# Kernel optimization log

Hardware: AMD Instinct MI355X
Metric: run time of the kernel (lower is better)

Reference implementation:

```python
import jax, jax.numpy as jnp
import numpy as np

N5, N4, N3, K = 10242, 2562, 642, 7  # icosphere node counts (levels 5,4,3), spatial kernel size
M = 32  # mchannel
EPS = 1e-8


def _sconv(x, neigh, W, b, relu=True):
    # x: [B,T,N,Cin]; neigh: [N,K] 1-ring indices; W: [K,Cin,Cout]
    xn = x[:, :, neigh, :]                        # [B,T,N,K,Cin] irregular gather
    y = jnp.einsum('btnkc,kcd->btnd', xn, W) + b  # per-node kernel contraction
    return jax.nn.relu(y) if relu else y


def _spool(x, pidx):
    # max-pool fine->coarse mesh: pidx [Ncoarse,Kp] indexes fine nodes
    return jnp.max(x[:, :, pidx, :], axis=3)


def _unpool(x, uidx):
    # coarse->fine copy: uidx [Nfine] indexes coarse nodes
    return x[:, :, uidx, :]


def _cos(f, a):
    # torch.nn.CosineSimilarity(dim=-1): dot / max(|f|*|a|, eps)
    dot = jnp.sum(f * a, axis=-1)
    nf = jnp.linalg.norm(f, axis=-1)
    na = jnp.linalg.norm(a, axis=-1)
    return dot / jnp.maximum(nf * na, EPS)


def setup_inputs() -> dict:
    key = jax.random.key(0)
    ks = jax.random.split(key, 32)
    w = lambda i, shape: jax.random.normal(ks[i], shape, jnp.float32) * 0.05
    inp = {
        'frame': jax.random.normal(ks[0], (1, 16, N5, 3), jnp.float32),
        'aem': jax.random.normal(ks[1], (1, 16, N5), jnp.float32),
        'W0f': w(2, (K, 3, M)),        'b0f': w(3, (M,)),
        'W0a': w(4, (K, 1, M)),        'b0a': w(5, (M,)),
        'W1f': w(6, (K, M, 2 * M)),    'b1f': w(7, (2 * M,)),
        'W1a': w(8, (K, M, 2 * M)),    'b1a': w(9, (2 * M,)),
        'W2f': w(10, (K, 2 * M, 4 * M)), 'b2f': w(11, (4 * M,)),
        'W2a': w(12, (K, 2 * M, 4 * M)), 'b2a': w(13, (4 * M,)),
        'W7': w(14, (K, 12 * M, 2 * M)), 'b7': w(15, (2 * M,)),
        'W8': w(16, (K, 4 * M, M)),    'b8': w(17, (M,)),
        'W9': w(18, (K, M, 1)),        'b9': w(19, (1,)),
        'neigh5': jax.random.randint(ks[20], (N5, K), 0, N5),
        'neigh4': jax.random.randint(ks[21], (N4, K), 0, N4),
        'neigh3': jax.random.randint(ks[22], (N3, K), 0, N3),
        'pool5': jax.random.randint(ks[23], (N4, K), 0, N5),
        'pool4': jax.random.randint(ks[24], (N3, K), 0, N4),
        'up4': jax.random.randint(ks[25], (N4,), 0, N3),
        'up5': jax.random.randint(ks[26], (N5,), 0, N4),
        'Tlocation': jax.random.randint(ks[27], (1, 16), 0, 16),
    }
    return inp


def reference(frame, aem, W0f, b0f, W0a, b0a, W1f, b1f, W1a, b1a, W2f, b2f,
              W2a, b2a, W7, b7, W8, b8, W9, b9,
              neigh5, neigh4, neigh3, pool5, pool4, up4, up5, Tlocation):
    a = aem[..., None]                                    # [B,T,N5,1]
    # encoder level 0 (N5)
    c0f = _sconv(frame, neigh5, W0f, b0f)
    c0a = _sconv(a, neigh5, W0a, b0a)
    p0f = _spool(c0f, pool5)
    p0a = _spool(c0a, pool5)
    m0 = _cos(c0f, c0a)[..., None]                        # [B,T,N5,1]
    c0f_att, c0a_att = c0f * m0, c0a * m0
    # encoder level 1 (N4)
    c1f = _sconv(p0f, neigh4, W1f, b1f)
    c1a = _sconv(p0a, neigh4, W1a, b1a)
    p1f = _spool(c1f, pool4)
    p1a = _spool(c1a, pool4)
    m1 = _cos(c1f, c1a)[..., None]
    c1f_att, c1a_att = c1f * m1, c1a * m1
    # bottleneck (N3)
    c2f = _sconv(p1f, neigh3, W2f, b2f)
    c2a = _sconv(p1a, neigh3, W2a, b2a)
    m2 = _cos(c2f, c2a)[..., None]
    conv2 = jnp.concatenate((c2f * m2, c2a * m2), axis=-1)  # [B,T,N3,8M]
    # decoder
    cat7 = jnp.concatenate((_unpool(conv2, up4), c1f_att, c1a_att), axis=-1)  # [B,T,N4,12M]
    conv7 = _sconv(cat7, neigh4, W7, b7)
    cat8 = jnp.concatenate((_unpool(conv7, up5), c0f_att, c0a_att), axis=-1)  # [B,T,N5,4M]
    conv8 = _sconv(cat8, neigh5, W8, b8)
    conv9 = _sconv(conv8, neigh5, W9, b9, relu=False)[..., 0]  # [B,T,N5]
    return jax.nn.softmax(conv9, axis=-1)
```

## Files before the change

kernel.cpp:

```cpp
#include <hip/hip_runtime.h>
#include <cfloat>
#include <cstdint>


constexpr int T  = 16;
constexpr int n5 = 10242, n4 = 2562, n3 = 642;
constexpr int K  = 7;

using bf16x8 = __attribute__((ext_vector_type(8))) short;
using f32x4  = __attribute__((ext_vector_type(4))) float;

static __device__ __forceinline__ float bf2f(unsigned short u) {
    return __uint_as_float((unsigned)u << 16);
}
static __device__ __forceinline__ unsigned short f2bf(float x) {
    unsigned u = __float_as_uint(x);
    u += 0x7FFF + ((u >> 16) & 1);
    return (unsigned short)(u >> 16);
}

__global__ __launch_bounds__(256) void conv0_kernel(
    const float* __restrict__ frame, const float* __restrict__ aem,
    const float* __restrict__ W0f, const float* __restrict__ b0f,
    const float* __restrict__ W0a, const float* __restrict__ b0a,
    const int* __restrict__ neigh5,
    unsigned short* __restrict__ c0f, unsigned short* __restrict__ c0a,
    unsigned short* __restrict__ att0)
{
    const int g = threadIdx.x >> 5;
    const int d = threadIdx.x & 31;
    const int per_t = (n5 + 7) / 8;
    const int t = blockIdx.x / per_t;
    const int n = (blockIdx.x % per_t) * 8 + g;
    if (n >= n5) return;

    float accf = b0f[d];
    float acca = b0a[d];
    const int* nb = neigh5 + n * K;
    #pragma unroll
    for (int k = 0; k < K; ++k) {
        const int j = nb[k];
        const float* fr = frame + ((size_t)t * n5 + j) * 3;
        const float av = aem[(size_t)t * n5 + j];
        accf = fmaf(fr[0], W0f[(k * 3 + 0) * 32 + d], accf);
        accf = fmaf(fr[1], W0f[(k * 3 + 1) * 32 + d], accf);
        accf = fmaf(fr[2], W0f[(k * 3 + 2) * 32 + d], accf);
        acca = fmaf(av, W0a[k * 32 + d], acca);
    }
    accf = fmaxf(accf, 0.f);
    acca = fmaxf(acca, 0.f);

    float dot = accf * acca, ff = accf * accf, aa = acca * acca;
    #pragma unroll
    for (int m = 1; m < 32; m <<= 1) {
        dot += __shfl_xor(dot, m, 32);
        ff  += __shfl_xor(ff,  m, 32);
        aa  += __shfl_xor(aa,  m, 32);
    }
    const float mm = dot / fmaxf(sqrtf(ff) * sqrtf(aa), 1e-8f);
    const size_t base = ((size_t)t * n5 + n) * 32;
    c0f[base + d] = f2bf(accf);
    c0a[base + d] = f2bf(acca);
    const size_t abase = ((size_t)t * n5 + n) * 64;
    att0[abase + d]      = f2bf(accf * mm);
    att0[abase + 32 + d] = f2bf(acca * mm);
}

template<int C>
__global__ __launch_bounds__(256) void pool_kernel(
    const unsigned short* __restrict__ in, const int* __restrict__ pidx,
    int Nin, int Nout, unsigned short* __restrict__ out)
{
    constexpr int C8 = C / 8;
    const int idx = blockIdx.x * 256 + threadIdx.x;
    if (idx >= T * Nout * C8) return;
    const int c8 = idx % C8;
    const int n  = (idx / C8) % Nout;
    const int t  = idx / (C8 * Nout);
    const int* pp = pidx + n * K;
    float m[8];
    #pragma unroll
    for (int j = 0; j < 8; ++j) m[j] = -FLT_MAX;
    #pragma unroll
    for (int k = 0; k < K; ++k) {
        const uint4 v = reinterpret_cast<const uint4*>(in)[((size_t)t * Nin + pp[k]) * C8 + c8];
        const unsigned short* s = reinterpret_cast<const unsigned short*>(&v);
        #pragma unroll
        for (int j = 0; j < 8; ++j) m[j] = fmaxf(m[j], bf2f(s[j]));
    }
    unsigned short o[8];
    #pragma unroll
    for (int j = 0; j < 8; ++j) o[j] = f2bf(m[j]);
    reinterpret_cast<uint4*>(out)[((size_t)t * Nout + n) * C8 + c8] =
        *reinterpret_cast<const uint4*>(o);
}

template<int C, int NN>
__global__ __launch_bounds__(256) void cosatt_kernel(
    const unsigned short* __restrict__ f, const unsigned short* __restrict__ a,
    unsigned short* __restrict__ att)
{
    constexpr int CPL = C / 64;
    const int w = threadIdx.x >> 6, lane = threadIdx.x & 63;
    const int idx = blockIdx.x * 4 + w;
    if (idx >= T * NN) return;
    const unsigned short* fr = f + (size_t)idx * C;
    const unsigned short* ar = a + (size_t)idx * C;
    float xs[CPL], ys[CPL];
    float dot = 0.f, ff = 0.f, aa = 0.f;
    #pragma unroll
    for (int i = 0; i < CPL; ++i) {
        const float x = bf2f(fr[lane + i * 64]);
        const float y = bf2f(ar[lane + i * 64]);
        xs[i] = x; ys[i] = y;
        dot = fmaf(x, y, dot);
        ff  = fmaf(x, x, ff);
        aa  = fmaf(y, y, aa);
    }
    #pragma unroll
    for (int msk = 1; msk < 64; msk <<= 1) {
        dot += __shfl_xor(dot, msk);
        ff  += __shfl_xor(ff,  msk);
        aa  += __shfl_xor(aa,  msk);
    }
    const float m = dot / fmaxf(sqrtf(ff) * sqrtf(aa), 1e-8f);
    unsigned short* orow = att + (size_t)idx * 2 * C;
    #pragma unroll
    for (int i = 0; i < CPL; ++i) {
        orow[lane + i * 64]     = f2bf(xs[i] * m);
        orow[C + lane + i * 64] = f2bf(ys[i] * m);
    }
}

struct PlainB16 {
    const unsigned short* x; int N; int C8;
    __device__ __forceinline__ uint4 row8(int t, int node, int c8) const {
        return reinterpret_cast<const uint4*>(x)[((size_t)t * N + node) * C8 + c8];
    }
};

struct Cat7B16 {
    const unsigned short* att2; const unsigned short* att1; const int* up4;
    __device__ __forceinline__ uint4 row8(int t, int node, int c8) const {
        if (c8 < 32)
            return reinterpret_cast<const uint4*>(att2)[((size_t)t * n3 + up4[node]) * 32 + c8];
        return reinterpret_cast<const uint4*>(att1)[((size_t)t * n4 + node) * 16 + (c8 - 32)];
    }
};

struct Cat8B16 {
    const unsigned short* cv7; const unsigned short* att0; const int* up5;
    __device__ __forceinline__ uint4 row8(int t, int node, int c8) const {
        if (c8 < 8)
            return reinterpret_cast<const uint4*>(cv7)[((size_t)t * n4 + up5[node]) * 8 + c8];
        return reinterpret_cast<const uint4*>(att0)[((size_t)t * n5 + node) * 8 + (c8 - 8)];
    }
};

__global__ __launch_bounds__(256) void wprep_all_kernel(
    const float* __restrict__ W1f, const float* __restrict__ W1a,
    const float* __restrict__ W2f, const float* __restrict__ W2a,
    const float* __restrict__ W7,  const float* __restrict__ W8,
    unsigned short* __restrict__ Wt1f, unsigned short* __restrict__ Wt1a,
    unsigned short* __restrict__ Wt2f, unsigned short* __restrict__ Wt2a,
    unsigned short* __restrict__ Wt7,  unsigned short* __restrict__ Wt8)
{
    int idx = blockIdx.x * 256 + threadIdx.x;
    const float* W; unsigned short* Wt; int KCv, CO;
    if (idx < 14336)       { W = W1f; Wt = Wt1f; KCv = 224;  CO = 64;  }
    else if (idx < 28672)  { idx -= 14336;  W = W1a; Wt = Wt1a; KCv = 224;  CO = 64;  }
    else if (idx < 86016)  { idx -= 28672;  W = W2f; Wt = Wt2f; KCv = 448;  CO = 128; }
    else if (idx < 143360) { idx -= 86016;  W = W2a; Wt = Wt2a; KCv = 448;  CO = 128; }
    else if (idx < 315392) { idx -= 143360; W = W7;  Wt = Wt7;  KCv = 2688; CO = 64;  }
    else                   { idx -= 315392; W = W8;  Wt = Wt8;  KCv = 896;  CO = 32;  }
    const int d = idx / KCv, kc = idx - d * KCv;
    Wt[idx] = f2bf(W[(size_t)kc * CO + d]);
}

template<int CIN, int COUT, int BM, int BK, class Loader>
__global__ __launch_bounds__(256) void sconv_mfma_kernel(
    Loader ldr, const int* __restrict__ neigh, int N, int tiles,
    const unsigned short* __restrict__ Wt, const float* __restrict__ bias,
    unsigned short* __restrict__ out)
{
    constexpr int KC = K * CIN, CHUNKS = CIN / BK, NK = K * CHUNKS;
    constexpr int WC = COUT / 32 <= 4 ? COUT / 32 : 4;
    constexpr int U4R = BK / 8;
    constexpr int VPTA = BM * U4R / 256;
    constexpr int VPTW = COUT * U4R / 256;
    static_assert(BM * COUT == 4096 && CIN % BK == 0 && VPTA >= 1 && VPTW >= 1);

    __shared__ __align__(16) unsigned short As[BM * BK];
    __shared__ __align__(16) unsigned short Ws[COUT * BK];
    __shared__ int nbs[K][BM];

    const int l = blockIdx.x;
    const int j = l >> 3;
    const int hi = (j >= tiles) ? 1 : 0;
    const int t  = 2 * (l & 7) + hi;
    const int n0 = (j - hi * tiles) * BM;

    const int tid  = threadIdx.x;
    const int lane = tid & 63, wave = tid >> 6;
    const int wr = wave / WC, wcol = wave % WC;
    const int l15 = lane & 15, lhi = lane >> 4;

    for (int i = tid; i < K * BM; i += 256) {
        const int r = i / K, k = i - r * K;
        nbs[k][r] = neigh[min(n0 + r, N - 1) * K + k];
    }

    f32x4 acc[2][2] = {};
    __syncthreads();

    for (int kt = 0; kt < NK; ++kt) {
        const int k   = kt / CHUNKS;
        const int cb8 = (kt - k * CHUNKS) * U4R;

        uint4 av[VPTA];
        #pragma unroll
        for (int v = 0; v < VPTA; ++v) {
            const int g = tid + v * 256, row = g / U4R, c8 = g % U4R;
            av[v] = ldr.row8(t, nbs[k][row], cb8 + c8);
        }
        uint4 wv[VPTW];
        #pragma unroll
        for (int v = 0; v < VPTW; ++v) {
            const int g = tid + v * 256, d = g / U4R, c8 = g % U4R;
            wv[v] = *reinterpret_cast<const uint4*>(Wt + (size_t)d * KC + kt * BK + c8 * 8);
        }

        __syncthreads();
        #pragma unroll
        for (int v = 0; v < VPTA; ++v) {
            const int g = tid + v * 256, row = g / U4R, c8 = g % U4R;
            *reinterpret_cast<uint4*>(&As[(row * BK + c8 * 8) ^ ((row & (U4R - 1)) << 3)]) = av[v];
        }
        #pragma unroll
        for (int v = 0; v < VPTW; ++v) {
            const int g = tid + v * 256, d = g / U4R, c8 = g % U4R;
            *reinterpret_cast<uint4*>(&Ws[(d * BK + c8 * 8) ^ ((d & (U4R - 1)) << 3)]) = wv[v];
        }
        __syncthreads();

        #pragma unroll
        for (int kk = 0; kk < BK / 32; ++kk) {
            const int kb = kk * 32 + lhi * 8;
            bf16x8 a[2], b[2];
            #pragma unroll
            for (int m = 0; m < 2; ++m) {
                const int row = wr * 32 + m * 16 + l15;
                a[m] = *reinterpret_cast<const bf16x8*>(
                    &As[(row * BK + kb) ^ ((row & (U4R - 1)) << 3)]);
            }
            #pragma unroll
            for (int n = 0; n < 2; ++n) {
                const int col = wcol * 32 + n * 16 + l15;
                b[n] = *reinterpret_cast<const bf16x8*>(
                    &Ws[(col * BK + kb) ^ ((col & (U4R - 1)) << 3)]);
            }
            #pragma unroll
            for (int m = 0; m < 2; ++m)
                #pragma unroll
                for (int n = 0; n < 2; ++n)
                    acc[m][n] = __builtin_amdgcn_mfma_f32_16x16x32_bf16(a[m], b[n], acc[m][n], 0, 0, 0);
        }
    }

    #pragma unroll
    for (int n = 0; n < 2; ++n) {
        const int gcol = wcol * 32 + n * 16 + l15;
        const float bv = bias[gcol];
        #pragma unroll
        for (int m = 0; m < 2; ++m) {
            #pragma unroll
            for (int i = 0; i < 4; ++i) {
                const int grow = n0 + wr * 32 + m * 16 + lhi * 4 + i;
                if (grow < N)
                    out[((size_t)t * N + grow) * COUT + gcol] =
                        f2bf(fmaxf(acc[m][n][i] + bv, 0.f));
            }
        }
    }
}

__global__ __launch_bounds__(256) void conv9_kernel(
    const unsigned short* __restrict__ cv8, const int* __restrict__ neigh5,
    const float* __restrict__ W9, const float* __restrict__ b9,
    float* __restrict__ logits)
{
    const int idx = blockIdx.x * 256 + threadIdx.x;
    if (idx >= T * n5) return;
    const int n = idx % n5;
    const int t = idx / n5;
    float acc = b9[0];
    const int* nb = neigh5 + n * K;
    #pragma unroll
    for (int k = 0; k < K; ++k) {
        const uint4* row = reinterpret_cast<const uint4*>(cv8 + ((size_t)t * n5 + nb[k]) * 32);
        const float* wk = W9 + k * 32;
        #pragma unroll
        for (int c4 = 0; c4 < 4; ++c4) {
            const uint4 v = row[c4];
            const unsigned short* s = reinterpret_cast<const unsigned short*>(&v);
            #pragma unroll
            for (int jj = 0; jj < 8; ++jj)
                acc = fmaf(bf2f(s[jj]), wk[c4 * 8 + jj], acc);
        }
    }
    logits[idx] = acc;
}

__global__ __launch_bounds__(1024) void softmax_kernel(
    const float* __restrict__ logits, float* __restrict__ out)
{
    const int t = blockIdx.x, tid = threadIdx.x;
    const float* x = logits + (size_t)t * n5;
    float* y = out + (size_t)t * n5;
    __shared__ float redmax[16], redsum[16];

    float mx = -FLT_MAX;
    for (int i = tid; i < n5; i += 1024) mx = fmaxf(mx, x[i]);
    #pragma unroll
    for (int m = 1; m < 64; m <<= 1) mx = fmaxf(mx, __shfl_xor(mx, m));
    if ((tid & 63) == 0) redmax[tid >> 6] = mx;
    __syncthreads();
    mx = redmax[0];
    #pragma unroll
    for (int i = 1; i < 16; ++i) mx = fmaxf(mx, redmax[i]);

    float s = 0.f;
    for (int i = tid; i < n5; i += 1024) s += expf(x[i] - mx);
    #pragma unroll
    for (int m = 1; m < 64; m <<= 1) s += __shfl_xor(s, m);
    if ((tid & 63) == 0) redsum[tid >> 6] = s;
    __syncthreads();
    s = 0.f;
    #pragma unroll
    for (int i = 0; i < 16; ++i) s += redsum[i];

    for (int i = tid; i < n5; i += 1024) y[i] = expf(x[i] - mx) / s;
}

extern "C" void kernel_launch(void* const* d_in, const int* in_sizes, int n_in,
                              void* d_out, int out_size, void* d_ws, size_t ws_size,
                              hipStream_t stream)
{
    const float* frame = (const float*)d_in[0];
    const float* aem   = (const float*)d_in[1];
    const float* W0f = (const float*)d_in[2];
    const float* b0f = (const float*)d_in[3];
    const float* W0a = (const float*)d_in[4];
    const float* b0a = (const float*)d_in[5];
    const float* W1f = (const float*)d_in[6];
    const float* b1f = (const float*)d_in[7];
    const float* W1a = (const float*)d_in[8];
    const float* b1a = (const float*)d_in[9];
    const float* W2f = (const float*)d_in[10];
    const float* b2f = (const float*)d_in[11];
    const float* W2a = (const float*)d_in[12];
    const float* b2a = (const float*)d_in[13];
    const float* W7  = (const float*)d_in[14];
    const float* b7  = (const float*)d_in[15];
    const float* W8  = (const float*)d_in[16];
    const float* b8  = (const float*)d_in[17];
    const float* W9  = (const float*)d_in[18];
    const float* b9  = (const float*)d_in[19];
    const int* neigh5 = (const int*)d_in[20];
    const int* neigh4 = (const int*)d_in[21];
    const int* neigh3 = (const int*)d_in[22];
    const int* pool5  = (const int*)d_in[23];
    const int* pool4  = (const int*)d_in[24];
    const int* up4    = (const int*)d_in[25];
    const int* up5    = (const int*)d_in[26];

    unsigned short* wsu = (unsigned short*)d_ws;
    size_t off = 0;
    auto ua = [&](size_t n) {
        unsigned short* p = wsu + off; off += (n + 7) & ~(size_t)7; return p;
    };
    unsigned short* c0f  = ua((size_t)T * n5 * 32);
    unsigned short* c0a  = ua((size_t)T * n5 * 32);
    unsigned short* att0 = ua((size_t)T * n5 * 64);
    unsigned short* p0f  = ua((size_t)T * n4 * 32);
    unsigned short* p0a  = ua((size_t)T * n4 * 32);
    unsigned short* c1f  = ua((size_t)T * n4 * 64);
    unsigned short* c1a  = ua((size_t)T * n4 * 64);
    unsigned short* att1 = ua((size_t)T * n4 * 128);
    unsigned short* p1f  = ua((size_t)T * n3 * 64);
    unsigned short* p1a  = ua((size_t)T * n3 * 64);
    unsigned short* c2f  = ua((size_t)T * n3 * 128);
    unsigned short* c2a  = ua((size_t)T * n3 * 128);
    unsigned short* att2 = ua((size_t)T * n3 * 256);
    unsigned short* cv7  = ua((size_t)T * n4 * 64);
    unsigned short* cv8  = ua((size_t)T * n5 * 32);
    unsigned short* Wt1f = ua((size_t)64 * 224);
    unsigned short* Wt1a = ua((size_t)64 * 224);
    unsigned short* Wt2f = ua((size_t)128 * 448);
    unsigned short* Wt2a = ua((size_t)128 * 448);
    unsigned short* Wt7  = ua((size_t)64 * 2688);
    unsigned short* Wt8  = ua((size_t)32 * 896);
    float* lgt = (float*)(wsu + off);

    wprep_all_kernel<<<1344, 256, 0, stream>>>(
        W1f, W1a, W2f, W2a, W7, W8, Wt1f, Wt1a, Wt2f, Wt2a, Wt7, Wt8);

    conv0_kernel<<<T * ((n5 + 7) / 8), 256, 0, stream>>>(
        frame, aem, W0f, b0f, W0a, b0a, neigh5, c0f, c0a, att0);

    {
        const int thr = T * n4 * (32 / 8);
        pool_kernel<32><<<(thr + 255) / 256, 256, 0, stream>>>(c0f, pool5, n5, n4, p0f);
        pool_kernel<32><<<(thr + 255) / 256, 256, 0, stream>>>(c0a, pool5, n5, n4, p0a);
    }

    constexpr int tiles1 = (n4 + 63) / 64;
    sconv_mfma_kernel<32, 64, 64, 32><<<T * tiles1, 256, 0, stream>>>(
        PlainB16{p0f, n4, 4}, neigh4, n4, tiles1, Wt1f, b1f, c1f);
    sconv_mfma_kernel<32, 64, 64, 32><<<T * tiles1, 256, 0, stream>>>(
        PlainB16{p0a, n4, 4}, neigh4, n4, tiles1, Wt1a, b1a, c1a);
    cosatt_kernel<64, n4><<<(T * n4 + 3) / 4, 256, 0, stream>>>(c1f, c1a, att1);

    {
        const int thr = T * n3 * (64 / 8);
        pool_kernel<64><<<(thr + 255) / 256, 256, 0, stream>>>(c1f, pool4, n4, n3, p1f);
        pool_kernel<64><<<(thr + 255) / 256, 256, 0, stream>>>(c1a, pool4, n4, n3, p1a);
    }

    constexpr int tiles2 = (n3 + 31) / 32;
    sconv_mfma_kernel<64, 128, 32, 64><<<T * tiles2, 256, 0, stream>>>(
        PlainB16{p1f, n3, 8}, neigh3, n3, tiles2, Wt2f, b2f, c2f);
    sconv_mfma_kernel<64, 128, 32, 64><<<T * tiles2, 256, 0, stream>>>(
        PlainB16{p1a, n3, 8}, neigh3, n3, tiles2, Wt2a, b2a, c2a);
    cosatt_kernel<128, n3><<<(T * n3 + 3) / 4, 256, 0, stream>>>(c2f, c2a, att2);

    constexpr int tiles7 = (n4 + 63) / 64;
    sconv_mfma_kernel<384, 64, 64, 64><<<T * tiles7, 256, 0, stream>>>(
        Cat7B16{att2, att1, up4}, neigh4, n4, tiles7, Wt7, b7, cv7);

    constexpr int tiles8 = (n5 + 127) / 128;
    sconv_mfma_kernel<128, 32, 128, 64><<<T * tiles8, 256, 0, stream>>>(
        Cat8B16{cv7, att0, up5}, neigh5, n5, tiles8, Wt8, b8, cv8);

    conv9_kernel<<<(T * n5 + 255) / 256, 256, 0, stream>>>(cv8, neigh5, W9, b9, lgt);

    softmax_kernel<<<T, 1024, 0, stream>>>(lgt, (float*)d_out);
}
```

Measured before the change: 323.7 us.

## Replace shared-memory tiled MFMA conv with per-wave register-direct gather MFMA

Rewrites the spherical conv kernel so each wave independently owns a 32x32 output tile and loads gathered activations and weights straight from global memory into MFMA operands. The shared-memory staging, neighbor table in LDS, and block-level __syncthreads are removed. The aim is lower sync and LDS overhead and finer-grained parallelism. In exchange, operand reuse across waves in a block is lost, so global and cache traffic for weights and gathered rows rises.

After: 357.9 us. +10.6%, slower.

```diff
diff --git a/kernel.cpp b/kernel.cpp
--- a/kernel.cpp
+++ b/kernel.cpp
@@ -177,105 +177,64 @@
     Wt[idx] = f2bf(W[(size_t)kc * CO + d]);
 }
 
-template<int CIN, int COUT, int BM, int BK, class Loader>
-__global__ __launch_bounds__(256) void sconv_mfma_kernel(
-    Loader ldr, const int* __restrict__ neigh, int N, int tiles,
+template<int CIN, int COUT, class Loader>
+__global__ __launch_bounds__(256) void sconv_rd_kernel(
+    Loader ldr, const int* __restrict__ neigh, int N, int Bt,
     const unsigned short* __restrict__ Wt, const float* __restrict__ bias,
     unsigned short* __restrict__ out)
 {
-    constexpr int KC = K * CIN, CHUNKS = CIN / BK, NK = K * CHUNKS;
-    constexpr int WC = COUT / 32 <= 4 ? COUT / 32 : 4;
-    constexpr int U4R = BK / 8;
-    constexpr int VPTA = BM * U4R / 256;
-    constexpr int VPTW = COUT * U4R / 256;
-    static_assert(BM * COUT == 4096 && CIN % BK == 0 && VPTA >= 1 && VPTW >= 1);
-
-    __shared__ __align__(16) unsigned short As[BM * BK];
-    __shared__ __align__(16) unsigned short Ws[COUT * BK];
-    __shared__ int nbs[K][BM];
-
-    const int l = blockIdx.x;
-    const int j = l >> 3;
-    const int hi = (j >= tiles) ? 1 : 0;
-    const int t  = 2 * (l & 7) + hi;
-    const int n0 = (j - hi * tiles) * BM;
-
-    const int tid  = threadIdx.x;
-    const int lane = tid & 63, wave = tid >> 6;
-    const int wr = wave / WC, wcol = wave % WC;
+    constexpr int KC = K * CIN;
+    constexpr int CHUNKS = CIN / 32;
+    constexpr int TN = COUT / 32;
+
+    const int wave = threadIdx.x >> 6;
+    const int lane = threadIdx.x & 63;
     const int l15 = lane & 15, lhi = lane >> 4;
 
-    for (int i = tid; i < K * BM; i += 256) {
-        const int r = i / K, k = i - r * K;
-        nbs[k][r] = neigh[min(n0 + r, N - 1) * K + k];
-    }
+    const int bj = blockIdx.x >> 3;
+    const int hi = (bj >= Bt) ? 1 : 0;
+    const int t  = 2 * (blockIdx.x & 7) + hi;
+    const int w  = (bj - hi * Bt) * 4 + wave;
+    const int TM = (N + 31) >> 5;
+    if (w >= TM * TN) return;
+    const int tile_n = w % TN, tile_m = w / TN;
+
+    const int r0 = tile_m * 32 + l15;
+    const int nrow0 = min(r0, N - 1) * K;
+    const int nrow1 = min(r0 + 16, N - 1) * K;
+
+    const int col0 = tile_n * 32 + l15;
+    const unsigned short* w0p = Wt + (size_t)col0 * KC + lhi * 8;
+    const unsigned short* w1p = w0p + (size_t)16 * KC;
 
     f32x4 acc[2][2] = {};
-    __syncthreads();
-
-    for (int kt = 0; kt < NK; ++kt) {
-        const int k   = kt / CHUNKS;
-        const int cb8 = (kt - k * CHUNKS) * U4R;
-
-        uint4 av[VPTA];
+
+    #pragma unroll
+    for (int k = 0; k < K; ++k) {
+        const int nb0 = neigh[nrow0 + k];
+        const int nb1 = neigh[nrow1 + k];
         #pragma unroll
-        for (int v = 0; v < VPTA; ++v) {
-            const int g = tid + v * 256, row = g / U4R, c8 = g % U4R;
-            av[v] = ldr.row8(t, nbs[k][row], cb8 + c8);
+        for (int c = 0; c < CHUNKS; ++c) {
+            const bf16x8 a0 = __builtin_bit_cast(bf16x8, ldr.row8(t, nb0, c * 4 + lhi));
+            const bf16x8 a1 = __builtin_bit_cast(bf16x8, ldr.row8(t, nb1, c * 4 + lhi));
+            const bf16x8 b0 = *reinterpret_cast<const bf16x8*>(w0p + k * CIN + c * 32);
+            const bf16x8 b1 = *reinterpret_cast<const bf16x8*>(w1p + k * CIN + c * 32);
+            acc[0][0] = __builtin_amdgcn_mfma_f32_16x16x32_bf16(a0, b0, acc[0][0], 0, 0, 0);
+            if (TN > 0) acc[0][1] = __builtin_amdgcn_mfma_f32_16x16x32_bf16(a0, b1, acc[0][1], 0, 0, 0);
+            acc[1][0] = __builtin_amdgcn_mfma_f32_16x16x32_bf16(a1, b0, acc[1][0], 0, 0, 0);
+            acc[1][1] = __builtin_amdgcn_mfma_f32_16x16x32_bf16(a1, b1, acc[1][1], 0, 0, 0);
         }
-        uint4 wv[VPTW];
-        #pragma unroll
-        for (int v = 0; v < VPTW; ++v) {
-            const int g = tid + v * 256, d = g / U4R, c8 = g % U4R;
-            wv[v] = *reinterpret_cast<const uint4*>(Wt + (size_t)d * KC + kt * BK + c8 * 8);
-        }
-
-        __syncthreads();
-        #pragma unroll
-        for (int v = 0; v < VPTA; ++v) {
-            const int g = tid + v * 256, row = g / U4R, c8 = g % U4R;
-            *reinterpret_cast<uint4*>(&As[(row * BK + c8 * 8) ^ ((row & (U4R - 1)) << 3)]) = av[v];
-        }
-        #pragma unroll
-        for (int v = 0; v < VPTW; ++v) {
-            const int g = tid + v * 256, d = g / U4R, c8 = g % U4R;
-            *reinterpret_cast<uint4*>(&Ws[(d * BK + c8 * 8) ^ ((d & (U4R - 1)) << 3)]) = wv[v];
-        }
-        __syncthreads();
-
-        #pragma unroll
-        for (int kk = 0; kk < BK / 32; ++kk) {
-            const int kb = kk * 32 + lhi * 8;
-            bf16x8 a[2], b[2];
-            #pragma unroll
-            for (int m = 0; m < 2; ++m) {
-                const int row = wr * 32 + m * 16 + l15;
-                a[m] = *reinterpret_cast<const bf16x8*>(
-                    &As[(row * BK + kb) ^ ((row & (U4R - 1)) << 3)]);
-            }
-            #pragma unroll
-            for (int n = 0; n < 2; ++n) {
-                const int col = wcol * 32 + n * 16 + l15;
-                b[n] = *reinterpret_cast<const bf16x8*>(
-                    &Ws[(col * BK + kb) ^ ((col & (U4R - 1)) << 3)]);
-            }
-            #pragma unroll
-            for (int m = 0; m < 2; ++m)
-                #pragma unroll
-                for (int n = 0; n < 2; ++n)
-                    acc[m][n] = __builtin_amdgcn_mfma_f32_16x16x32_bf16(a[m], b[n], acc[m][n], 0, 0, 0);
-        }
     }
 
     #pragma unroll
     for (int n = 0; n < 2; ++n) {
-        const int gcol = wcol * 32 + n * 16 + l15;
+        const int gcol = tile_n * 32 + n * 16 + l15;
         const float bv = bias[gcol];
         #pragma unroll
         for (int m = 0; m < 2; ++m) {
             #pragma unroll
             for (int i = 0; i < 4; ++i) {
-                const int grow = n0 + wr * 32 + m * 16 + lhi * 4 + i;
+                const int grow = tile_m * 32 + m * 16 + lhi * 4 + i;
                 if (grow < N)
                     out[((size_t)t * N + grow) * COUT + gcol] =
                         f2bf(fmaxf(acc[m][n][i] + bv, 0.f));
@@ -414,11 +373,13 @@
         pool_kernel<32><<<(thr + 255) / 256, 256, 0, stream>>>(c0a, pool5, n5, n4, p0a);
     }
 
-    constexpr int tiles1 = (n4 + 63) / 64;
-    sconv_mfma_kernel<32, 64, 64, 32><<<T * tiles1, 256, 0, stream>>>(
-        PlainB16{p0f, n4, 4}, neigh4, n4, tiles1, Wt1f, b1f, c1f);
-    sconv_mfma_kernel<32, 64, 64, 32><<<T * tiles1, 256, 0, stream>>>(
-        PlainB16{p0a, n4, 4}, neigh4, n4, tiles1, Wt1a, b1a, c1a);
+    {
+        constexpr int Bt = (81 * 2 + 3) / 4;
+        sconv_rd_kernel<32, 64><<<16 * Bt, 256, 0, stream>>>(
+            PlainB16{p0f, n4, 4}, neigh4, n4, Bt, Wt1f, b1f, c1f);
+        sconv_rd_kernel<32, 64><<<16 * Bt, 256, 0, stream>>>(
+            PlainB16{p0a, n4, 4}, neigh4, n4, Bt, Wt1a, b1a, c1a);
+    }
     cosatt_kernel<64, n4><<<(T * n4 + 3) / 4, 256, 0, stream>>>(c1f, c1a, att1);
 
     {
@@ -427,20 +388,26 @@
         pool_kernel<64><<<(thr + 255) / 256, 256, 0, stream>>>(c1a, pool4, n4, n3, p1a);
     }
 
-    constexpr int tiles2 = (n3 + 31) / 32;
-    sconv_mfma_kernel<64, 128, 32, 64><<<T * tiles2, 256, 0, stream>>>(
-        PlainB16{p1f, n3, 8}, neigh3, n3, tiles2, Wt2f, b2f, c2f);
-    sconv_mfma_kernel<64, 128, 32, 64><<<T * tiles2, 256, 0, stream>>>(
-        PlainB16{p1a, n3, 8}, neigh3, n3, tiles2, Wt2a, b2a, c2a);
+    {
+        constexpr int Bt = (21 * 4 + 3) / 4;
+        sconv_rd_kernel<64, 128><<<16 * Bt, 256, 0, stream>>>(
+            PlainB16{p1f, n3, 8}, neigh3, n3, Bt, Wt2f, b2f, c2f);
+        sconv_rd_kernel<64, 128><<<16 * Bt, 256, 0, stream>>>(
+            PlainB16{p1a, n3, 8}, neigh3, n3, Bt, Wt2a, b2a, c2a);
+    }
     cosatt_kernel<128, n3><<<(T * n3 + 3) / 4, 256, 0, stream>>>(c2f, c2a, att2);
 
-    constexpr int tiles7 = (n4 + 63) / 64;
-    sconv_mfma_kernel<384, 64, 64, 64><<<T * tiles7, 256, 0, stream>>>(
-        Cat7B16{att2, att1, up4}, neigh4, n4, tiles7, Wt7, b7, cv7);
-
-    constexpr int tiles8 = (n5 + 127) / 128;
-    sconv_mfma_kernel<128, 32, 128, 64><<<T * tiles8, 256, 0, stream>>>(
-        Cat8B16{cv7, att0, up5}, neigh5, n5, tiles8, Wt8, b8, cv8);
+    {
+        constexpr int Bt = (81 * 2 + 3) / 4;
+        sconv_rd_kernel<384, 64><<<16 * Bt, 256, 0, stream>>>(
+            Cat7B16{att2, att1, up4}, neigh4, n4, Bt, Wt7, b7, cv7);
+    }
+
+    {
+        constexpr int Bt = (321 * 1 + 3) / 4;
+        sconv_rd_kernel<128, 32><<<16 * Bt, 256, 0, stream>>>(
+            Cat8B16{cv7, att0, up5}, neigh5, n5, Bt, Wt8, b8, cv8);
+    }
 
     conv9_kernel<<<(T * n5 + 255) / 256, 256, 0, stream>>>(cv8, neigh5, W9, b9, lgt);
 
```
